# Optimization experiments

Measured on AMD Instinct MI355X. Metric: run time of the kernel, lower is better.

Reference implementation:

```python
import jax, jax.numpy as jnp
import numpy as np

EPS = 1e-12  # matches torch F.normalize default eps


def _l2_normalize(x):
    # F.normalize: x / max(||x||_2, eps), along last dim
    n = jnp.sqrt(jnp.sum(x * x, axis=-1, keepdims=True))
    return x / jnp.maximum(n, EPS)


def setup_inputs() -> dict:
    key = jax.random.key(0)
    k1, k2, k3, k4 = jax.random.split(key, 4)
    N, M, D = 2048, 100000, 256
    return {
        "shape_embedding": jax.random.normal(k1, (N, D), dtype=jnp.float32),
        "gallery_embedding": jax.random.normal(k2, (M, D), dtype=jnp.float32),
        "category_idx": jax.random.randint(k3, (M,), 0, 9, dtype=jnp.int64) if jax.config.jax_enable_x64 else jax.random.randint(k3, (M,), 0, 9, dtype=jnp.int32),
        "shape_idx": jax.random.randint(k4, (M,), 0, 10000, dtype=jnp.int32),
    }


def reference(shape_embedding, gallery_embedding, category_idx, shape_idx):
    # Gallery embeddings are L2-normalized once in __init__; query normalized per call.
    g = _l2_normalize(gallery_embedding)          # [M, D]
    q = _l2_normalize(shape_embedding)            # [N, D]
    scores = jnp.einsum('nd,md->nm', q, g)        # cosine similarity [N, M]
    idx = jnp.argmax(scores, axis=-1)             # top-1 retrieval [N]
    return category_idx[idx], shape_idx[idx]
```

## Files before the change

### kernel.cpp

```cpp
#include <hip/hip_runtime.h>
#include <hip/hip_fp16.h>
#include <math.h>
#include <float.h>

#define M_G 100000
#define M_PAD 100096
#define NMT 782
#define N_Q 2048
#define DIM 256
#define NG 3128
#define GSTR 3136
#define MARGIN 0.009f

typedef _Float16 f16x8 __attribute__((ext_vector_type(8)));
typedef float f32x4 __attribute__((ext_vector_type(4)));

#define WS_GP 0
#define WS_QP 51249152
#define WS_BM 52297728

__device__ inline unsigned pack_h2(float a, float b) {
    __half ha = __float2half(a), hb = __float2half(b);
    return (unsigned)*(unsigned short*)&ha | ((unsigned)*(unsigned short*)&hb << 16);
}
__device__ inline void gload_lds16(const void* gsrc, void* ldst) {
    __builtin_amdgcn_global_load_lds(
        (const __attribute__((address_space(1))) unsigned int*)gsrc,
        (__attribute__((address_space(3))) unsigned int*)ldst, 16, 0, 0);
}

#define BAR __builtin_amdgcn_s_barrier()
#define LGKM0 { asm volatile("s_waitcnt lgkmcnt(0)" ::: "memory"); \
                __builtin_amdgcn_sched_barrier(0); }
#define VMCNT(n) { asm volatile("s_waitcnt vmcnt(" #n ")" ::: "memory"); \
                   __builtin_amdgcn_sched_barrier(0); }

__global__ __launch_bounds__(256) void pack_kernel(
    const float* __restrict__ g, const float* __restrict__ q,
    uint4* __restrict__ gp, uint4* __restrict__ qp)
{
    const int b = blockIdx.x;
    const int w4 = threadIdx.x >> 6, lane = threadIdx.x & 63;
    const bool isg = b < (M_PAD / 4);
    const int row = (isg ? b : b - M_PAD / 4) * 4 + w4;
    const bool real = !isg || row < M_G;
    const float* src = isg ? g + (size_t)row * DIM : q + (size_t)row * DIM;

    float inv = 0.0f;
    if (real) {
        float4 v = ((const float4*)src)[lane];
        float ss = v.x * v.x + v.y * v.y + v.z * v.z + v.w * v.w;
        #pragma unroll
        for (int o = 32; o; o >>= 1) ss += __shfl_xor(ss, o);
        inv = 1.0f / fmaxf(sqrtf(ss), 1e-12f);
    }
    if (lane < 32) {
        uint4 w = make_uint4(0u, 0u, 0u, 0u);
        if (real) {
            float4 a = ((const float4*)src)[lane * 2];
            float4 c = ((const float4*)src)[lane * 2 + 1];
            w.x = pack_h2(a.x * inv, a.y * inv);
            w.y = pack_h2(a.z * inv, a.w * inv);
            w.z = pack_h2(c.x * inv, c.y * inv);
            w.w = pack_h2(c.z * inv, c.w * inv);
        }
        const int kt = lane >> 3, gg = lane & 7;
        if (isg) {
            int mt = row >> 7, rl = row & 127;
            gp[((size_t)mt * 4 + kt) * 1024 + rl * 8 + (gg ^ (rl & 7))] = w;
        } else {
            int qt = row >> 8, rl = row & 255;
            qp[((size_t)qt * 4 + kt) * 2048 + rl * 8 + (gg ^ (rl & 7))] = w;
        }
    }
}

#define STAGE64(dstbase, src) { const uint4* s_ = (src); _Pragma("unroll") \
  for (int p_ = 0; p_ < 8; ++p_) \
    gload_lds16(s_ + p_ * 512 + tid, lds + (dstbase) + (p_ * 512 + tid) * 16); }

#define STAGE_QALL { _Pragma("unroll") \
  for (int c_ = 0; c_ < 16; ++c_) \
    gload_lds16(qsrc + c_ * 512 + tid, lds + (c_ * 512 + tid) * 16); }

#define READ_BP(KT, bufbase) { _Pragma("unroll") \
  for (int nj = 0; nj < 4; ++nj) { \
    const char* p_ = lds + (bufbase) + (wc * 64 + nj * 16 + r16) * 128; \
    bR[KT][0][nj] = *(const f16x8*)(p_ + sw0); \
    bR[KT][1][nj] = *(const f16x8*)(p_ + sw1); } }

__global__ __launch_bounds__(512, 2) void scoreA_kernel(
    const uint4* __restrict__ gp, const uint4* __restrict__ qp,
    unsigned short* __restrict__ bmaxH)
{
    extern __shared__ char lds[];

    const int bid = blockIdx.x;
    const int qt = bid >> 5, mc = bid & 31;
    const int nt = (mc < 14) ? 25 : 24;
    const int t0 = (mc < 14) ? mc * 25 : 350 + (mc - 14) * 24;

    const int tid = threadIdx.x;
    const int wid = tid >> 6, lane = tid & 63;
    const int wr = wid >> 2, wc = wid & 3;
    const int r16 = lane & 15, rhi = lane >> 4;
    const int sw0 = ((rhi ^ (r16 & 7)) << 4);
    const int sw1 = (((4 + rhi) ^ (r16 & 7)) << 4);

    const uint4* qsrc = qp + (size_t)qt * 8192;

    f16x8 bR[4][2][4];
    STAGE_QALL;
    VMCNT(0); BAR;
    READ_BP(0, 0); READ_BP(1, 32768); READ_BP(2, 65536); READ_BP(3, 98304);
    LGKM0; BAR;
    STAGE64(0, gp + (size_t)t0 * 4096);
    VMCNT(0); BAR;

    for (int t = 0; t < nt; ++t) {
        const int mtile = t0 + t;
        const int cur = (t & 1) << 16;
        const int nxt = cur ^ 65536;
        if (t + 1 < nt) STAGE64(nxt, gp + (size_t)(mtile + 1) * 4096);

        f32x4 acc[4][4];
        #pragma unroll
        for (int f = 0; f < 4; ++f)
            #pragma unroll
            for (int nj = 0; nj < 4; ++nj) acc[f][nj] = (f32x4){0.f, 0.f, 0.f, 0.f};

        #pragma unroll
        for (int kt = 0; kt < 4; ++kt) {
            #pragma unroll
            for (int kk = 0; kk < 2; ++kk) {
                const char* pbase = lds + cur + kt * 16384;
                const int sw = kk ? sw1 : sw0;
                f16x8 aR[4];
                #pragma unroll
                for (int f = 0; f < 4; ++f) {
                    int row = wr * 64 + f * 16 + r16;
                    aR[f] = *(const f16x8*)(pbase + row * 128 + sw);
                }
                #pragma unroll
                for (int f = 0; f < 4; ++f)
                    #pragma unroll
                    for (int nj = 0; nj < 4; ++nj)
                        acc[f][nj] = __builtin_amdgcn_mfma_f32_16x16x32_f16(
                            aR[f], bR[kt][kk][nj], acc[f][nj], 0, 0, 0);
            }
        }

        #pragma unroll
        for (int gidx = 0; gidx < 2; ++gidx) {
            float cm[4] = {-FLT_MAX, -FLT_MAX, -FLT_MAX, -FLT_MAX};
            #pragma unroll
            for (int fo = 0; fo < 2; ++fo) {
                int f = gidx * 2 + fo;
                #pragma unroll
                for (int jj = 0; jj < 4; ++jj)
                    #pragma unroll
                    for (int nj = 0; nj < 4; ++nj)
                        cm[nj] = fmaxf(cm[nj], acc[f][nj][jj]);
            }
            const int group = mtile * 4 + wr * 2 + gidx;
            const bool padgrp = (mtile * 128 + (wr * 2 + gidx) * 32) >= M_G;
            #pragma unroll
            for (int nj = 0; nj < 4; ++nj) {
                float v = cm[nj];
                v = fmaxf(v, __shfl_xor(v, 16));
                v = fmaxf(v, __shfl_xor(v, 32));
                if (lane < 16) {
                    int qn = qt * 256 + wc * 64 + nj * 16 + lane;
                    __half h = __float2half(padgrp ? -65504.f : v);
                    bmaxH[(size_t)qn * GSTR + group] = *(unsigned short*)&h;
                }
            }
        }
        if (t + 1 < nt) { VMCNT(8); BAR; }
    }
}

__global__ __launch_bounds__(256) void phaseB_kernel(
    const float* __restrict__ q, const float* __restrict__ g,
    const unsigned short* __restrict__ bmaxH,
    const int* __restrict__ cat, const int* __restrict__ shp,
    int* __restrict__ out)
{
    __shared__ __align__(16) float qrow[DIM];
    __shared__ int glist[NG];
    __shared__ int ng;
    __shared__ float smax[4];
    __shared__ float rbs[4];
    __shared__ int rbi[4];

    const int qi = blockIdx.x;
    const int tid = threadIdx.x;
    const int lane = tid & 63, wid = tid >> 6;
    const __half* bm = (const __half*)(bmaxH + (size_t)qi * GSTR);
    if (tid < 64)
        *(float4*)&qrow[tid * 4] = *(const float4*)(q + (size_t)qi * DIM + tid * 4);
    if (tid == 0) ng = 0;

    float m = -FLT_MAX;
    for (int gr = tid; gr < NG; gr += 256)
        m = fmaxf(m, __half2float(bm[gr]));
    #pragma unroll
    for (int o = 32; o; o >>= 1) m = fmaxf(m, __shfl_xor(m, o));
    if (lane == 0) smax[wid] = m;
    __syncthreads();
    const float thr = fmaxf(fmaxf(smax[0], smax[1]), fmaxf(smax[2], smax[3])) - MARGIN;

    for (int gr = tid; gr < NG; gr += 256)
        if (__half2float(bm[gr]) >= thr)
            glist[atomicAdd(&ng, 1)] = gr;
    __syncthreads();

    float bs = -FLT_MAX;
    int bi = 0x7fffffff;
    const int r = tid >> 3, p = tid & 7;
    const int n = ng;
    for (int i = 0; i < n; ++i) {
        int mm = glist[i] * 32 + r;
        if (mm < M_G) {
            const float* grow = g + (size_t)mm * DIM + p * 32;
            const float* qr = qrow + p * 32;
            float s = 0.f, ssq = 0.f;
            #pragma unroll
            for (int jj = 0; jj < 8; ++jj) {
                float4 gv = *(const float4*)(grow + jj * 4);
                float4 qv = *(const float4*)(qr + jj * 4);
                s += gv.x * qv.x + gv.y * qv.y + gv.z * qv.z + gv.w * qv.w;
                ssq += gv.x * gv.x + gv.y * gv.y + gv.z * gv.z + gv.w * gv.w;
            }
            s += __shfl_xor(s, 1);  s += __shfl_xor(s, 2);  s += __shfl_xor(s, 4);
            ssq += __shfl_xor(ssq, 1); ssq += __shfl_xor(ssq, 2); ssq += __shfl_xor(ssq, 4);
            s *= 1.0f / fmaxf(sqrtf(ssq), 1e-12f);
            if (p == 0 && (s > bs || (s == bs && mm < bi))) { bs = s; bi = mm; }
        }
    }
    #pragma unroll
    for (int o = 1; o < 64; o <<= 1) {
        float os = __shfl_xor(bs, o);
        int oi = __shfl_xor(bi, o);
        if (os > bs || (os == bs && oi < bi)) { bs = os; bi = oi; }
    }
    if (lane == 0) { rbs[wid] = bs; rbi[wid] = bi; }
    __syncthreads();
    if (tid == 0) {
        #pragma unroll
        for (int ww = 1; ww < 4; ++ww)
            if (rbs[ww] > bs || (rbs[ww] == bs && rbi[ww] < bi)) { bs = rbs[ww]; bi = rbi[ww]; }
        out[qi] = cat[bi];
        out[N_Q + qi] = shp[bi];
    }
}

extern "C" void kernel_launch(void* const* d_in, const int* in_sizes, int n_in,
                              void* d_out, int out_size, void* d_ws, size_t ws_size,
                              hipStream_t stream) {
    const float* q = (const float*)d_in[0];
    const float* g = (const float*)d_in[1];
    const int* cat = (const int*)d_in[2];
    const int* shp = (const int*)d_in[3];
    int* out = (int*)d_out;

    char* ws = (char*)d_ws;
    uint4* gp             = (uint4*)(ws + WS_GP);
    uint4* qp             = (uint4*)(ws + WS_QP);
    unsigned short* bmaxH = (unsigned short*)(ws + WS_BM);

    hipFuncSetAttribute((const void*)scoreA_kernel,
                        hipFuncAttributeMaxDynamicSharedMemorySize, 131072);

    pack_kernel<<<M_PAD / 4 + N_Q / 4, 256, 0, stream>>>(g, q, gp, qp);
    scoreA_kernel<<<256, 512, 131072, stream>>>(gp, qp, bmaxH);
    phaseB_kernel<<<N_Q, 256, 0, stream>>>(q, g, bmaxH, cat, shp, out);
}
```

Before: 168.2 us.

## Shrink score tiles to 64 gallery rows with 256-thread blocks and XCD-aware mapping

The gallery tile drops from 128 to 64 rows, giving 4 waves per block instead of 8 and halving LDS to 64KB. The grid doubles to 512 blocks, and block IDs are mapped so blocks sharing an XCD work on neighbouring gallery chunks. The query slice is now staged through the two 32KB buffers in sequence. The aim is more resident blocks per CU and better L2 locality, at the cost of less reuse of each gallery tile across waves and more loads and barriers per MFMA.

```diff
diff --git a/kernel.cpp b/kernel.cpp
--- a/kernel.cpp
+++ b/kernel.cpp
@@ -4,11 +4,11 @@
 #include <float.h>
 
 #define M_G 100000
-#define M_PAD 100096
-#define NMT 782
+#define M_PAD 100032
+#define NT64 1563
 #define N_Q 2048
 #define DIM 256
-#define NG 3128
+#define NG 3126
 #define GSTR 3136
 #define MARGIN 0.009f
 
@@ -16,8 +16,8 @@
 typedef float f32x4 __attribute__((ext_vector_type(4)));
 
 #define WS_GP 0
-#define WS_QP 51249152
-#define WS_BM 52297728
+#define WS_QP 51216384
+#define WS_BM 52264960
 
 __device__ inline unsigned pack_h2(float a, float b) {
     __half ha = __float2half(a), hb = __float2half(b);
@@ -66,8 +66,8 @@
         }
         const int kt = lane >> 3, gg = lane & 7;
         if (isg) {
-            int mt = row >> 7, rl = row & 127;
-            gp[((size_t)mt * 4 + kt) * 1024 + rl * 8 + (gg ^ (rl & 7))] = w;
+            int mt = row >> 6, rl = row & 63;
+            gp[((size_t)mt * 4 + kt) * 512 + rl * 8 + (gg ^ (rl & 7))] = w;
         } else {
             int qt = row >> 8, rl = row & 255;
             qp[((size_t)qt * 4 + kt) * 2048 + rl * 8 + (gg ^ (rl & 7))] = w;
@@ -75,13 +75,9 @@
     }
 }
 
-#define STAGE64(dstbase, src) { const uint4* s_ = (src); _Pragma("unroll") \
+#define STAGE32K(dstbase, src) { const uint4* s_ = (src); _Pragma("unroll") \
   for (int p_ = 0; p_ < 8; ++p_) \
-    gload_lds16(s_ + p_ * 512 + tid, lds + (dstbase) + (p_ * 512 + tid) * 16); }
-
-#define STAGE_QALL { _Pragma("unroll") \
-  for (int c_ = 0; c_ < 16; ++c_) \
-    gload_lds16(qsrc + c_ * 512 + tid, lds + (c_ * 512 + tid) * 16); }
+    gload_lds16(s_ + p_ * 256 + tid, lds + (dstbase) + (p_ * 256 + tid) * 16); }
 
 #define READ_BP(KT, bufbase) { _Pragma("unroll") \
   for (int nj = 0; nj < 4; ++nj) { \
@@ -89,20 +85,21 @@
     bR[KT][0][nj] = *(const f16x8*)(p_ + sw0); \
     bR[KT][1][nj] = *(const f16x8*)(p_ + sw1); } }
 
-__global__ __launch_bounds__(512, 2) void scoreA_kernel(
+__global__ __launch_bounds__(256, 2) void scoreA_kernel(
     const uint4* __restrict__ gp, const uint4* __restrict__ qp,
     unsigned short* __restrict__ bmaxH)
 {
     extern __shared__ char lds[];
 
     const int bid = blockIdx.x;
-    const int qt = bid >> 5, mc = bid & 31;
-    const int nt = (mc < 14) ? 25 : 24;
-    const int t0 = (mc < 14) ? mc * 25 : 350 + (mc - 14) * 24;
+    const int xcd = bid & 7;
+    const int qt = (bid >> 3) & 7;
+    const int mc = (bid >> 6) * 8 + xcd;
+    const int nt = (mc < 27) ? 25 : 24;
+    const int t0 = (mc < 27) ? mc * 25 : 675 + (mc - 27) * 24;
 
     const int tid = threadIdx.x;
-    const int wid = tid >> 6, lane = tid & 63;
-    const int wr = wid >> 2, wc = wid & 3;
+    const int wc = tid >> 6, lane = tid & 63;
     const int r16 = lane & 15, rhi = lane >> 4;
     const int sw0 = ((rhi ^ (r16 & 7)) << 4);
     const int sw1 = (((4 + rhi) ^ (r16 & 7)) << 4);
@@ -110,18 +107,26 @@
     const uint4* qsrc = qp + (size_t)qt * 8192;
 
     f16x8 bR[4][2][4];
-    STAGE_QALL;
-    VMCNT(0); BAR;
-    READ_BP(0, 0); READ_BP(1, 32768); READ_BP(2, 65536); READ_BP(3, 98304);
-    LGKM0; BAR;
-    STAGE64(0, gp + (size_t)t0 * 4096);
+    STAGE32K(0,     qsrc + 0 * 2048);
+    STAGE32K(32768, qsrc + 1 * 2048);
+    VMCNT(8); BAR;
+    READ_BP(0, 0); LGKM0; BAR;
+    STAGE32K(0, qsrc + 2 * 2048);
+    VMCNT(8); BAR;
+    READ_BP(1, 32768); LGKM0; BAR;
+    STAGE32K(32768, qsrc + 3 * 2048);
+    VMCNT(8); BAR;
+    READ_BP(2, 0); LGKM0; BAR;
+    STAGE32K(0, gp + (size_t)t0 * 2048);
+    VMCNT(8); BAR;
+    READ_BP(3, 32768); LGKM0; BAR;
     VMCNT(0); BAR;
 
     for (int t = 0; t < nt; ++t) {
         const int mtile = t0 + t;
-        const int cur = (t & 1) << 16;
-        const int nxt = cur ^ 65536;
-        if (t + 1 < nt) STAGE64(nxt, gp + (size_t)(mtile + 1) * 4096);
+        const int cur = (t & 1) << 15;
+        const int nxt = cur ^ 32768;
+        if (t + 1 < nt) STAGE32K(nxt, gp + (size_t)(mtile + 1) * 2048);
 
         f32x4 acc[4][4];
         #pragma unroll
@@ -133,14 +138,12 @@
         for (int kt = 0; kt < 4; ++kt) {
             #pragma unroll
             for (int kk = 0; kk < 2; ++kk) {
-                const char* pbase = lds + cur + kt * 16384;
+                const char* pbase = lds + cur + kt * 8192;
                 const int sw = kk ? sw1 : sw0;
                 f16x8 aR[4];
                 #pragma unroll
-                for (int f = 0; f < 4; ++f) {
-                    int row = wr * 64 + f * 16 + r16;
-                    aR[f] = *(const f16x8*)(pbase + row * 128 + sw);
-                }
+                for (int f = 0; f < 4; ++f)
+                    aR[f] = *(const f16x8*)(pbase + (f * 16 + r16) * 128 + sw);
                 #pragma unroll
                 for (int f = 0; f < 4; ++f)
                     #pragma unroll
@@ -162,8 +165,8 @@
                     for (int nj = 0; nj < 4; ++nj)
                         cm[nj] = fmaxf(cm[nj], acc[f][nj][jj]);
             }
-            const int group = mtile * 4 + wr * 2 + gidx;
-            const bool padgrp = (mtile * 128 + (wr * 2 + gidx) * 32) >= M_G;
+            const int group = mtile * 2 + gidx;
+            const bool padgrp = (mtile * 64 + gidx * 32) >= M_G;
             #pragma unroll
             for (int nj = 0; nj < 4; ++nj) {
                 float v = cm[nj];
@@ -270,9 +273,9 @@
     unsigned short* bmaxH = (unsigned short*)(ws + WS_BM);
 
     hipFuncSetAttribute((const void*)scoreA_kernel,
-                        hipFuncAttributeMaxDynamicSharedMemorySize, 131072);
+                        hipFuncAttributeMaxDynamicSharedMemorySize, 65536);
 
     pack_kernel<<<M_PAD / 4 + N_Q / 4, 256, 0, stream>>>(g, q, gp, qp);
-    scoreA_kernel<<<256, 512, 131072, stream>>>(gp, qp, bmaxH);
+    scoreA_kernel<<<512, 256, 65536, stream>>>(gp, qp, bmaxH);
     phaseB_kernel<<<N_Q, 256, 0, stream>>>(q, g, bmaxH, cat, shp, out);
 }
```

New measurement: 166.3 us. About the same (-1.1%).
